# Kernel tuning notes

Hardware: AMD Instinct MI355X
Metric: run time of the kernel (lower is better)

The kernel has to match this reference:

```python
import jax, jax.numpy as jnp
import numpy as np

N = 100000
E = 6400000
GAMMA = 1.0
SUPPORT = 0.05


def cohesion_kernel(q, h):
    # piecewise Akinci cohesion kernel (Cd normalization is unused in the original)
    qm1_3_q3 = (q - 1.0) ** 3 * q ** 3
    k1 = 128.0 * qm1_3_q3 + 1.0   # q <= 0.5
    k2 = 64.0 * qm1_3_q3           # q > 0.5
    return -jnp.where(q <= 0.5, k1, k2)


def kernel_gradient(q, dist, h):
    # 2D Wendland C2 kernel gradient: W = 7/(pi h^2) (1-q)^4 (1+4q)
    C = 7.0 / (np.pi * h ** 2)
    dWdq = C * (-20.0 * q * jnp.clip(1.0 - q, 0.0, None) ** 3) / h
    return dWdq[:, None] * dist  # [E,2]


def setup_inputs() -> dict:
    key = jax.random.key(0)
    k1, k2, k3, k4, k5, k6, k7 = jax.random.split(key, 7)
    neighbors = jnp.stack([
        jax.random.randint(k1, (E,), 0, N),
        jax.random.randint(k2, (E,), 0, N),
    ], axis=0)  # [2,E] int
    fluidAreas = jax.random.uniform(k3, (N,), dtype=jnp.float32)
    fluidDensities = jax.random.uniform(k4, (N,), dtype=jnp.float32) + 0.5  # avoid div-by-0
    fluidRestDensity = jax.random.uniform(k5, (N,), dtype=jnp.float32) + 0.5
    fluidRadialDistances = jax.random.uniform(k6, (E,), dtype=jnp.float32)  # q in [0,1]
    fluidDistances = jax.random.normal(k7, (E, 2), dtype=jnp.float32)
    # normalize to unit direction vectors as in the SPH pipeline
    fluidDistances = fluidDistances / (jnp.linalg.norm(fluidDistances, axis=1, keepdims=True) + 1e-7)
    return {
        'neighbors': neighbors,
        'fluidAreas': fluidAreas,
        'fluidDensities': fluidDensities,
        'fluidRestDensity': fluidRestDensity,
        'fluidRadialDistances': fluidRadialDistances,
        'fluidDistances': fluidDistances,
    }


def reference(neighbors, fluidAreas, fluidDensities, fluidRestDensity,
              fluidRadialDistances, fluidDistances):
    i = neighbors[0]
    j = neighbors[1]

    # computeNormalFunction
    fac_n = fluidAreas[j] / fluidDensities[j]                  # [E]
    grad = kernel_gradient(fluidRadialDistances, fluidDistances, SUPPORT)  # [E,2]
    normals = SUPPORT * jax.ops.segment_sum(fac_n[:, None] * grad, i, num_segments=N)  # [N,2]

    # computeCurvatureForce
    curvature = -GAMMA * jax.ops.segment_sum(normals[i] - normals[j], i, num_segments=N)

    # computeCohesionForce
    fac_c = fluidAreas[j] * fluidRestDensity[j]                # [E]
    kern = cohesion_kernel(fluidRadialDistances, SUPPORT)      # [E]
    cohesion = -GAMMA * jax.ops.segment_sum((fac_c * kern)[:, None] * fluidDistances, i, num_segments=N)

    # both forces are accumulated into fluidAcceleration
    return curvature + cohesion
```

## Files before the change

### kernel.cpp

```cpp
#include <hip/hip_runtime.h>

constexpr int N_PART = 100000;
constexpr int N_EDGE = 6400000;
constexpr float SUPPORT = 0.05f;
constexpr float PI_F = 3.14159265358979323846f;

constexpr int CH_LOG2 = 12;
constexpr int CH      = 1 << CH_LOG2;
constexpr int NCH     = (N_EDGE + CH - 1) / CH;
constexpr int BIN_LOG2 = 12;
constexpr int BINSZ   = 1 << BIN_LOG2;
constexpr int NBIN    = (N_PART + BINSZ - 1) / BINSZ;
constexpr int BT_STRIDE = 32;
constexpr int G_MAX   = 40;
constexpr int ST_NW   = 8;
constexpr int MAXC    = 272;

__global__ __launch_bounds__(512) void prep_fac(
    const float* __restrict__ areas,
    const float* __restrict__ dens,
    const float* __restrict__ rest,
    float2* __restrict__ fac)
{
    int p = blockIdx.x * blockDim.x + threadIdx.x;
    if (p < N_PART)
        fac[p] = make_float2(areas[p] / dens[p], areas[p] * rest[p]);
}

__global__ __launch_bounds__(512) void l1_sort(
    const int* __restrict__ nb,
    const float2* __restrict__ fac,
    const float* __restrict__ q,
    const float2* __restrict__ dist,
    unsigned* __restrict__ gpack,
    float2* __restrict__ gpay1,
    float2* __restrict__ gpay2,
    unsigned* __restrict__ btab)
{
    __shared__ unsigned rec_pack[CH];
    __shared__ float    rec_q[CH];
    __shared__ float    rec_dx[CH];
    __shared__ float    rec_dy[CH];
    __shared__ unsigned hist[ST_NW * NBIN];
    __shared__ unsigned wbase[ST_NW * NBIN];
    __shared__ unsigned kpre[ST_NW * 8 * NBIN];
    __shared__ unsigned base[NBIN + 1];
    __shared__ unsigned bcnt[NBIN];

    const int t   = blockIdx.x;
    const int c0  = t * CH;
    const int len = min(CH, N_EDGE - c0);
    const int tid = threadIdx.x;
    const int wid = tid >> 6;
    const int lane = tid & 63;

    unsigned iv[8], jv[8];
    float    qv[8], dxv[8], dyv[8];
    #pragma unroll
    for (int k = 0; k < 8; ++k) {
        int idx = tid + k * 512;
        if (idx < len) {
            iv[k] = (unsigned)nb[c0 + idx];
            jv[k] = (unsigned)nb[N_EDGE + c0 + idx];
            qv[k] = q[c0 + idx];
            float2 d = dist[c0 + idx];
            dxv[k] = d.x;
            dyv[k] = d.y;
        }
    }

    unsigned rnk[8];
    unsigned cntb = 0;
    #pragma unroll
    for (int k = 0; k < 8; ++k) {
        int idx = tid + k * 512;
        unsigned bin = (idx < len) ? (iv[k] >> BIN_LOG2) : 0xFFu;
        if (lane < NBIN) kpre[(wid * 8 + k) * NBIN + lane] = cntb;
        unsigned r = 0;
        for (unsigned b = 0; b < (unsigned)NBIN; ++b) {
            unsigned long long m = __ballot(bin == b);
            unsigned lt = __builtin_amdgcn_mbcnt_hi((unsigned)(m >> 32),
                          __builtin_amdgcn_mbcnt_lo((unsigned)m, 0u));
            if (bin == b) r = lt;
            if ((unsigned)lane == b) cntb += (unsigned)__popcll(m);
        }
        rnk[k] = r;
    }
    if (lane < NBIN) hist[wid * NBIN + lane] = cntb;
    __syncthreads();

    if (tid < NBIN) {
        unsigned run = 0;
        for (int w = 0; w < ST_NW; ++w) {
            wbase[w * NBIN + tid] = run;
            run += hist[w * NBIN + tid];
        }
        bcnt[tid] = run;
    }
    __syncthreads();
    if (tid == 0) {
        unsigned run = 0;
        for (int b = 0; b < NBIN; ++b) { base[b] = run; run += bcnt[b]; }
        base[NBIN] = run;
    }
    __syncthreads();
    if (tid < ST_NW * NBIN) wbase[tid] += base[tid % NBIN];
    if (tid < NBIN)  btab[t * BT_STRIDE + tid]  = base[tid];
    if (tid == NBIN) btab[t * BT_STRIDE + NBIN] = (unsigned)len;
    __syncthreads();

    #pragma unroll
    for (int k = 0; k < 8; ++k) {
        int idx = tid + k * 512;
        if (idx < len) {
            unsigned i   = iv[k];
            unsigned bin = i >> BIN_LOG2;
            unsigned pos = (wbase[wid * NBIN + bin]
                          + kpre[(wid * 8 + k) * NBIN + bin]
                          + rnk[k]) & (CH - 1);
            rec_pack[pos] = ((i & (BINSZ - 1)) << 17) | jv[k];
            rec_q[pos]    = qv[k];
            rec_dx[pos]   = dxv[k];
            rec_dy[pos]   = dyv[k];
        }
    }
    __syncthreads();

    const float Cw = 7.0f / (PI_F * SUPPORT * SUPPORT);
    for (int p = tid; p < len; p += 512) {
        unsigned pack = rec_pack[p];
        float qq = rec_q[p];
        float dx = rec_dx[p], dy = rec_dy[p];
        unsigned j = pack & 0x1FFFFu;
        float2 f = fac[j];

        float omq  = fmaxf(1.0f - qq, 0.0f);
        float dWdq = Cw * (-20.0f * qq * omq * omq * omq) * (1.0f / SUPPORT);
        float s    = SUPPORT * f.x * dWdq;

        float qm1  = qq - 1.0f;
        float tt   = qm1 * qm1 * qm1 * qq * qq * qq;
        float kern = (qq <= 0.5f) ? fmaf(128.0f, tt, 1.0f) : 64.0f * tt;
        float fc   = f.y * kern;

        int o = c0 + p;
        gpack[o] = pack;
        gpay1[o] = make_float2(s * dx, s * dy);
        gpay2[o] = make_float2(fc * dx, fc * dy);
    }
}

__global__ __launch_bounds__(512) void passB(
    const unsigned* __restrict__ btab,
    const unsigned* __restrict__ gpack,
    const float2* __restrict__ gpay1,
    float2* __restrict__ partials,
    int G)
{
    __shared__ float accx[BINSZ];
    __shared__ float accy[BINSZ];
    __shared__ unsigned s_sb[MAXC], s_se[MAXC];
    const int b = blockIdx.x % NBIN;
    const int g = blockIdx.x / NBIN;
    const int wave = threadIdx.x >> 6;
    const int lane = threadIdx.x & 63;

    const int t0 = (int)((long long)g * NCH / G);
    const int t1 = (int)((long long)(g + 1) * NCH / G);
    const int nt = t1 - t0;

    for (int k = threadIdx.x; k < BINSZ; k += 512) { accx[k] = 0.0f; accy[k] = 0.0f; }
    for (int c = threadIdx.x; c < nt; c += 512) {
        s_sb[c] = btab[(t0 + c) * BT_STRIDE + b];
        s_se[c] = btab[(t0 + c) * BT_STRIDE + b + 1];
    }
    __syncthreads();

    for (int c = wave; c < nt; c += 8) {
        const int c0  = (t0 + c) * CH;
        unsigned sb = s_sb[c], se = s_se[c];
        unsigned k = sb + lane;
        for (; k + 64 < se; k += 128) {
            int o0 = c0 + (int)k, o1 = o0 + 64;
            unsigned pk0 = gpack[o0], pk1 = gpack[o1];
            float2 p0 = gpay1[o0], p1 = gpay1[o1];
            unsigned l0 = (pk0 >> 17) & (BINSZ - 1);
            unsigned l1 = (pk1 >> 17) & (BINSZ - 1);
            atomicAdd(&accx[l0], p0.x);
            atomicAdd(&accy[l0], p0.y);
            atomicAdd(&accx[l1], p1.x);
            atomicAdd(&accy[l1], p1.y);
        }
        if (k < se) {
            int o = c0 + (int)k;
            unsigned pk = gpack[o];
            float2 p = gpay1[o];
            unsigned loc = (pk >> 17) & (BINSZ - 1);
            atomicAdd(&accx[loc], p.x);
            atomicAdd(&accy[loc], p.y);
        }
    }
    __syncthreads();

    float2* __restrict__ dst = partials + (size_t)g * (NBIN * BINSZ) + (size_t)b * BINSZ;
    for (int k = threadIdx.x; k < BINSZ; k += 512)
        dst[k] = make_float2(accx[k], accy[k]);
}

__global__ __launch_bounds__(512) void passD(
    const unsigned* __restrict__ btab,
    const unsigned* __restrict__ gpack,
    const float2* __restrict__ gpay2,
    const float2* __restrict__ normals,
    float2* __restrict__ partials,
    int G)
{
    __shared__ float accx[BINSZ];
    __shared__ float accy[BINSZ];
    __shared__ unsigned s_sb[MAXC], s_se[MAXC];
    const int b = blockIdx.x % NBIN;
    const int g = blockIdx.x / NBIN;
    const int wave = threadIdx.x >> 6;
    const int lane = threadIdx.x & 63;

    const int t0 = (int)((long long)g * NCH / G);
    const int t1 = (int)((long long)(g + 1) * NCH / G);
    const int nt = t1 - t0;

    for (int k = threadIdx.x; k < BINSZ; k += 512) { accx[k] = 0.0f; accy[k] = 0.0f; }
    for (int c = threadIdx.x; c < nt; c += 512) {
        s_sb[c] = btab[(t0 + c) * BT_STRIDE + b];
        s_se[c] = btab[(t0 + c) * BT_STRIDE + b + 1];
    }
    __syncthreads();

    const int gbase = b * BINSZ;
    for (int c = wave; c < nt; c += 8) {
        const int c0  = (t0 + c) * CH;
        unsigned sb = s_sb[c], se = s_se[c];
        unsigned k = sb + lane;
        for (; k + 64 < se; k += 128) {
            int o0 = c0 + (int)k, o1 = o0 + 64;
            unsigned pk0 = gpack[o0], pk1 = gpack[o1];
            float2 h0 = gpay2[o0], h1 = gpay2[o1];
            unsigned j0 = min(pk0 & 0x1FFFFu, (unsigned)(N_PART - 1));
            unsigned j1 = min(pk1 & 0x1FFFFu, (unsigned)(N_PART - 1));
            unsigned l0 = (pk0 >> 17) & (BINSZ - 1);
            unsigned l1 = (pk1 >> 17) & (BINSZ - 1);
            unsigned i0 = min((unsigned)(gbase + l0), (unsigned)(N_PART - 1));
            unsigned i1 = min((unsigned)(gbase + l1), (unsigned)(N_PART - 1));
            float2 nj0 = normals[j0];
            float2 nj1 = normals[j1];
            float2 ni0 = normals[i0];
            float2 ni1 = normals[i1];
            atomicAdd(&accx[l0], nj0.x - ni0.x + h0.x);
            atomicAdd(&accy[l0], nj0.y - ni0.y + h0.y);
            atomicAdd(&accx[l1], nj1.x - ni1.x + h1.x);
            atomicAdd(&accy[l1], nj1.y - ni1.y + h1.y);
        }
        if (k < se) {
            int o = c0 + (int)k;
            unsigned pk = gpack[o];
            float2 coh = gpay2[o];
            unsigned j   = min(pk & 0x1FFFFu, (unsigned)(N_PART - 1));
            unsigned loc = (pk >> 17) & (BINSZ - 1);
            unsigned ii  = min((unsigned)(gbase + loc), (unsigned)(N_PART - 1));
            float2 nj = normals[j];
            float2 ni = normals[ii];
            atomicAdd(&accx[loc], nj.x - ni.x + coh.x);
            atomicAdd(&accy[loc], nj.y - ni.y + coh.y);
        }
    }
    __syncthreads();

    float2* __restrict__ dst = partials + (size_t)g * (NBIN * BINSZ) + (size_t)b * BINSZ;
    for (int k = threadIdx.x; k < BINSZ; k += 512)
        dst[k] = make_float2(accx[k], accy[k]);
}

__global__ __launch_bounds__(256) void reduceG(
    const float2* __restrict__ partials, float2* __restrict__ dst, int G)
{
    int p = blockIdx.x * blockDim.x + threadIdx.x;
    if (p >= N_PART) return;
    float ax = 0.0f, ay = 0.0f;
    for (int g = 0; g < G; ++g) {
        float2 v = partials[(size_t)g * (NBIN * BINSZ) + p];
        ax += v.x; ay += v.y;
    }
    dst[p] = make_float2(ax, ay);
}

constexpr int FB_BSZ_LOG2 = 13;
constexpr int FB_BSZ   = 1 << FB_BSZ_LOG2;
constexpr int FB_NBINS = (N_PART + FB_BSZ - 1) / FB_BSZ;
constexpr int FB_NP_PAD = FB_NBINS * FB_BSZ;
constexpr int FB_C_TARGET = 39;

__global__ __launch_bounds__(1024) void fb_pass1_binned(
    const int* __restrict__ nb, const float* __restrict__ areas,
    const float* __restrict__ dens, const float* __restrict__ q,
    const float2* __restrict__ dist, float* __restrict__ partials, int C)
{
    __shared__ float lds[2 * FB_BSZ];
    const int b = blockIdx.x % FB_NBINS;
    const int c = blockIdx.x / FB_NBINS;
    for (int k = threadIdx.x; k < 2 * FB_BSZ; k += blockDim.x) lds[k] = 0.0f;
    __syncthreads();
    const int start = (int)((long long)c       * (N_EDGE / 4) / C) * 4;
    const int end   = (int)((long long)(c + 1) * (N_EDGE / 4) / C) * 4;
    const int4* __restrict__ nb4 = (const int4*)nb;
    const float Cw = 7.0f / (PI_F * SUPPORT * SUPPORT);
    for (int e = start + (int)threadIdx.x * 4; e < end; e += (int)blockDim.x * 4) {
        int4 iq = nb4[e >> 2];
        #pragma unroll
        for (int k = 0; k < 4; ++k) {
            int iv = (k == 0) ? iq.x : (k == 1) ? iq.y : (k == 2) ? iq.z : iq.w;
            if ((iv >> FB_BSZ_LOG2) == b) {
                int ee = e + k;
                int j  = nb[N_EDGE + ee];
                float qq  = q[ee];
                float fac = areas[j] / dens[j];
                float omq  = fmaxf(1.0f - qq, 0.0f);
                float dWdq = Cw * (-20.0f * qq * omq * omq * omq) * (1.0f / SUPPORT);
                float s = SUPPORT * fac * dWdq;
                float2 d = dist[ee];
                int loc = (iv & (FB_BSZ - 1)) << 1;
                atomicAdd(&lds[loc],     s * d.x);
                atomicAdd(&lds[loc + 1], s * d.y);
            }
        }
    }
    __syncthreads();
    float2* __restrict__ dst = (float2*)partials + (size_t)c * FB_NP_PAD + (size_t)b * FB_BSZ;
    const float2* __restrict__ src = (const float2*)lds;
    for (int k = threadIdx.x; k < FB_BSZ; k += blockDim.x) dst[k] = src[k];
}

__global__ __launch_bounds__(1024) void fb_pass2_binned(
    const int* __restrict__ nb, const float* __restrict__ areas,
    const float* __restrict__ rest, const float* __restrict__ q,
    const float2* __restrict__ dist, const float2* __restrict__ normals,
    float* __restrict__ partials, int C)
{
    __shared__ float lds[2 * FB_BSZ];
    const int b = blockIdx.x % FB_NBINS;
    const int c = blockIdx.x / FB_NBINS;
    for (int k = threadIdx.x; k < 2 * FB_BSZ; k += blockDim.x) lds[k] = 0.0f;
    __syncthreads();
    const int start = (int)((long long)c       * (N_EDGE / 4) / C) * 4;
    const int end   = (int)((long long)(c + 1) * (N_EDGE / 4) / C) * 4;
    const int4* __restrict__ nb4 = (const int4*)nb;
    for (int e = start + (int)threadIdx.x * 4; e < end; e += (int)blockDim.x * 4) {
        int4 iq = nb4[e >> 2];
        #pragma unroll
        for (int k = 0; k < 4; ++k) {
            int iv = (k == 0) ? iq.x : (k == 1) ? iq.y : (k == 2) ? iq.z : iq.w;
            if ((iv >> FB_BSZ_LOG2) == b) {
                int ee = e + k;
                int j  = nb[N_EDGE + ee];
                float2 ni = normals[iv];
                float2 nj = normals[j];
                float qq  = q[ee];
                float fc  = areas[j] * rest[j];
                float qm1 = qq - 1.0f;
                float t   = qm1 * qm1 * qm1 * qq * qq * qq;
                float kern = (qq <= 0.5f) ? fmaf(128.0f, t, 1.0f) : 64.0f * t;
                float2 d = dist[ee];
                int loc = (iv & (FB_BSZ - 1)) << 1;
                atomicAdd(&lds[loc],     -(ni.x - nj.x) + fc * kern * d.x);
                atomicAdd(&lds[loc + 1], -(ni.y - nj.y) + fc * kern * d.y);
            }
        }
    }
    __syncthreads();
    float2* __restrict__ dst = (float2*)partials + (size_t)c * FB_NP_PAD + (size_t)b * FB_BSZ;
    const float2* __restrict__ src = (const float2*)lds;
    for (int k = threadIdx.x; k < FB_BSZ; k += blockDim.x) dst[k] = src[k];
}

__global__ __launch_bounds__(256) void fb_reduce_partials(
    const float* __restrict__ partials, float* __restrict__ dst, int C)
{
    int p = blockIdx.x * blockDim.x + threadIdx.x;
    if (p >= N_PART) return;
    const float2* __restrict__ p2 = (const float2*)partials;
    float ax = 0.0f, ay = 0.0f;
    for (int c = 0; c < C; ++c) {
        float2 v = p2[(size_t)c * FB_NP_PAD + p];
        ax += v.x; ay += v.y;
    }
    ((float2*)dst)[p] = make_float2(ax, ay);
}

__global__ __launch_bounds__(256) void fb_zero2(float* __restrict__ a,
                                                float* __restrict__ b, int n) {
    int idx = blockIdx.x * blockDim.x + threadIdx.x;
    if (idx < n) { a[idx] = 0.0f; b[idx] = 0.0f; }
}

__global__ __launch_bounds__(256) void fb_pass1_atomic(
    const int* __restrict__ nb, const float* __restrict__ areas,
    const float* __restrict__ dens, const float* __restrict__ q,
    const float2* __restrict__ dist, float* __restrict__ normals)
{
    int e = blockIdx.x * blockDim.x + threadIdx.x;
    if (e >= N_EDGE) return;
    int i = nb[e];
    int j = nb[N_EDGE + e];
    float qq  = q[e];
    float fac = areas[j] / dens[j];
    const float Cw = 7.0f / (PI_F * SUPPORT * SUPPORT);
    float omq  = fmaxf(1.0f - qq, 0.0f);
    float dWdq = Cw * (-20.0f * qq * omq * omq * omq) * (1.0f / SUPPORT);
    float s = SUPPORT * fac * dWdq;
    float2 d = dist[e];
    atomicAdd(&normals[2 * i],     s * d.x);
    atomicAdd(&normals[2 * i + 1], s * d.y);
}

__global__ __launch_bounds__(256) void fb_pass2_atomic(
    const int* __restrict__ nb, const float* __restrict__ areas,
    const float* __restrict__ rest, const float* __restrict__ q,
    const float2* __restrict__ dist, const float2* __restrict__ normals,
    float* __restrict__ out)
{
    int e = blockIdx.x * blockDim.x + threadIdx.x;
    if (e >= N_EDGE) return;
    int i = nb[e];
    int j = nb[N_EDGE + e];
    float2 ni = normals[i];
    float2 nj = normals[j];
    float qq  = q[e];
    float fc  = areas[j] * rest[j];
    float qm1 = qq - 1.0f;
    float t   = qm1 * qm1 * qm1 * qq * qq * qq;
    float kern = (qq <= 0.5f) ? fmaf(128.0f, t, 1.0f) : 64.0f * t;
    float2 d = dist[e];
    atomicAdd(&out[2 * i],     -(ni.x - nj.x) + fc * kern * d.x);
    atomicAdd(&out[2 * i + 1], -(ni.y - nj.y) + fc * kern * d.y);
}

extern "C" void kernel_launch(void* const* d_in, const int* in_sizes, int n_in,
                              void* d_out, int out_size, void* d_ws, size_t ws_size,
                              hipStream_t stream) {
    const int*   nb    = (const int*)d_in[0];
    const float* areas = (const float*)d_in[1];
    const float* dens  = (const float*)d_in[2];
    const float* rest  = (const float*)d_in[3];
    const float* q     = (const float*)d_in[4];
    const float* dist  = (const float*)d_in[5];
    float* out = (float*)d_out;

    size_t off = 0;
    auto take = [&](size_t bytes) { size_t o = off; off += (bytes + 255) & ~(size_t)255; return o; };
    size_t o_pack    = take((size_t)N_EDGE * sizeof(unsigned));
    size_t o_pay1    = take((size_t)N_EDGE * sizeof(float2));
    size_t o_pay2    = take((size_t)N_EDGE * sizeof(float2));
    size_t o_btab    = take((size_t)NCH * BT_STRIDE * sizeof(unsigned));
    size_t o_normals = take((size_t)N_PART * sizeof(float2));
    size_t o_fac     = take((size_t)N_PART * sizeof(float2));
    size_t base_need = off;
    const size_t per_g = (size_t)(NBIN * BINSZ) * sizeof(float2);

    int G = 0;
    if (ws_size > base_need) {
        G = (int)((ws_size - base_need) / per_g);
        if (G > G_MAX) G = G_MAX;
    }

    char* ws = (char*)d_ws;

    if (G >= 6) {
        unsigned* gpack   = (unsigned*)(ws + o_pack);
        float2*   gpay1   = (float2*)(ws + o_pay1);
        float2*   gpay2   = (float2*)(ws + o_pay2);
        unsigned* btab    = (unsigned*)(ws + o_btab);
        float2*   normals = (float2*)(ws + o_normals);
        float2*   fac     = (float2*)(ws + o_fac);
        float2*   partials= (float2*)(ws + base_need);

        prep_fac<<<(N_PART + 511) / 512, 512, 0, stream>>>(areas, dens, rest, fac);
        l1_sort<<<NCH, 512, 0, stream>>>(
            nb, fac, q, (const float2*)dist,
            gpack, gpay1, gpay2, btab);
        passB<<<NBIN * G, 512, 0, stream>>>(btab, gpack, gpay1, partials, G);
        reduceG<<<(N_PART + 255) / 256, 256, 0, stream>>>(partials, normals, G);
        passD<<<NBIN * G, 512, 0, stream>>>(btab, gpack, gpay2, normals, partials, G);
        reduceG<<<(N_PART + 255) / 256, 256, 0, stream>>>(partials, (float2*)out, G);
        return;
    }

    const size_t normals_pad = 1 << 20;
    float* normals  = (float*)d_ws;
    float* partials = (float*)((char*)d_ws + normals_pad);
    const size_t per_chunk = (size_t)FB_NP_PAD * 2 * sizeof(float);
    int C = 0;
    if (ws_size > normals_pad) {
        C = (int)((ws_size - normals_pad) / per_chunk);
        if (C > FB_C_TARGET) C = FB_C_TARGET;
    }

    if (C >= 4) {
        const int grid = FB_NBINS * C;
        fb_pass1_binned<<<grid, 1024, 0, stream>>>(
            nb, areas, dens, q, (const float2*)dist, partials, C);
        fb_reduce_partials<<<(N_PART + 255) / 256, 256, 0, stream>>>(partials, normals, C);
        fb_pass2_binned<<<grid, 1024, 0, stream>>>(
            nb, areas, rest, q, (const float2*)dist, (const float2*)normals, partials, C);
        fb_reduce_partials<<<(N_PART + 255) / 256, 256, 0, stream>>>(partials, out, C);
    } else {
        const int nv = 2 * N_PART;
        fb_zero2<<<(nv + 255) / 256, 256, 0, stream>>>(normals, out, nv);
        const int blocks = (N_EDGE + 255) / 256;
        fb_pass1_atomic<<<blocks, 256, 0, stream>>>(
            nb, areas, dens, q, (const float2*)dist, normals);
        fb_pass2_atomic<<<blocks, 256, 0, stream>>>(
            nb, areas, rest, q, (const float2*)dist, (const float2*)normals, out);
    }
}
```

Baseline: 384.7 us.

## Use LDS atomic ranking for bin scatter and pack records as float4

The per-chunk bin sort now ranks edges with shared-memory atomic counters instead of a 25-iteration ballot/mbcnt loop per element, which drops the kpre prefix table. The four separate shared arrays for pack, q, dx and dy become one float4 array, so each record is written and read with a single 16-byte access. The pass that accumulates into bins now unrolls its loads to four per lane to keep more memory requests in flight. The atomic ranking makes the order within a bin nondeterministic, which can change the float summation order, and the atomics may contend on hot bins.

```diff
diff --git a/kernel.cpp b/kernel.cpp
--- a/kernel.cpp
+++ b/kernel.cpp
@@ -37,13 +37,9 @@
     float2* __restrict__ gpay2,
     unsigned* __restrict__ btab)
 {
-    __shared__ unsigned rec_pack[CH];
-    __shared__ float    rec_q[CH];
-    __shared__ float    rec_dx[CH];
-    __shared__ float    rec_dy[CH];
+    __shared__ float4   rec[CH];
     __shared__ unsigned hist[ST_NW * NBIN];
-    __shared__ unsigned wbase[ST_NW * NBIN];
-    __shared__ unsigned kpre[ST_NW * 8 * NBIN];
+    __shared__ unsigned curw[ST_NW * NBIN];
     __shared__ unsigned base[NBIN + 1];
     __shared__ unsigned bcnt[NBIN];
 
@@ -52,7 +48,8 @@
     const int len = min(CH, N_EDGE - c0);
     const int tid = threadIdx.x;
     const int wid = tid >> 6;
-    const int lane = tid & 63;
+
+    for (int k = tid; k < ST_NW * NBIN; k += 512) hist[k] = 0u;
 
     unsigned iv[8], jv[8];
     float    qv[8], dxv[8], dyv[8];
@@ -68,31 +65,20 @@
             dyv[k] = d.y;
         }
     }
-
-    unsigned rnk[8];
-    unsigned cntb = 0;
+    __syncthreads();
+
     #pragma unroll
     for (int k = 0; k < 8; ++k) {
         int idx = tid + k * 512;
-        unsigned bin = (idx < len) ? (iv[k] >> BIN_LOG2) : 0xFFu;
-        if (lane < NBIN) kpre[(wid * 8 + k) * NBIN + lane] = cntb;
-        unsigned r = 0;
-        for (unsigned b = 0; b < (unsigned)NBIN; ++b) {
-            unsigned long long m = __ballot(bin == b);
-            unsigned lt = __builtin_amdgcn_mbcnt_hi((unsigned)(m >> 32),
-                          __builtin_amdgcn_mbcnt_lo((unsigned)m, 0u));
-            if (bin == b) r = lt;
-            if ((unsigned)lane == b) cntb += (unsigned)__popcll(m);
-        }
-        rnk[k] = r;
-    }
-    if (lane < NBIN) hist[wid * NBIN + lane] = cntb;
+        if (idx < len)
+            atomicAdd(&hist[wid * NBIN + (iv[k] >> BIN_LOG2)], 1u);
+    }
     __syncthreads();
 
     if (tid < NBIN) {
         unsigned run = 0;
         for (int w = 0; w < ST_NW; ++w) {
-            wbase[w * NBIN + tid] = run;
+            curw[w * NBIN + tid] = run;
             run += hist[w * NBIN + tid];
         }
         bcnt[tid] = run;
@@ -104,7 +90,7 @@
         base[NBIN] = run;
     }
     __syncthreads();
-    if (tid < ST_NW * NBIN) wbase[tid] += base[tid % NBIN];
+    if (tid < ST_NW * NBIN) curw[tid] += base[tid % NBIN];
     if (tid < NBIN)  btab[t * BT_STRIDE + tid]  = base[tid];
     if (tid == NBIN) btab[t * BT_STRIDE + NBIN] = (unsigned)len;
     __syncthreads();
@@ -115,22 +101,19 @@
         if (idx < len) {
             unsigned i   = iv[k];
             unsigned bin = i >> BIN_LOG2;
-            unsigned pos = (wbase[wid * NBIN + bin]
-                          + kpre[(wid * 8 + k) * NBIN + bin]
-                          + rnk[k]) & (CH - 1);
-            rec_pack[pos] = ((i & (BINSZ - 1)) << 17) | jv[k];
-            rec_q[pos]    = qv[k];
-            rec_dx[pos]   = dxv[k];
-            rec_dy[pos]   = dyv[k];
+            unsigned r = atomicAdd(&curw[wid * NBIN + bin], 1u) & (CH - 1);
+            unsigned pk = ((i & (BINSZ - 1)) << 17) | jv[k];
+            rec[r] = make_float4(__uint_as_float(pk), qv[k], dxv[k], dyv[k]);
         }
     }
     __syncthreads();
 
     const float Cw = 7.0f / (PI_F * SUPPORT * SUPPORT);
     for (int p = tid; p < len; p += 512) {
-        unsigned pack = rec_pack[p];
-        float qq = rec_q[p];
-        float dx = rec_dx[p], dy = rec_dy[p];
+        float4 v = rec[p];
+        unsigned pack = __float_as_uint(v.x);
+        float qq = v.y;
+        float dx = v.z, dy = v.w;
         unsigned j = pack & 0x1FFFFu;
         float2 f = fac[j];
 
@@ -180,18 +163,22 @@
         const int c0  = (t0 + c) * CH;
         unsigned sb = s_sb[c], se = s_se[c];
         unsigned k = sb + lane;
-        for (; k + 64 < se; k += 128) {
-            int o0 = c0 + (int)k, o1 = o0 + 64;
-            unsigned pk0 = gpack[o0], pk1 = gpack[o1];
-            float2 p0 = gpay1[o0], p1 = gpay1[o1];
+        for (; k + 192 < se; k += 256) {
+            int o0 = c0 + (int)k;
+            unsigned pk0 = gpack[o0], pk1 = gpack[o0 + 64],
+                     pk2 = gpack[o0 + 128], pk3 = gpack[o0 + 192];
+            float2 p0 = gpay1[o0],       p1 = gpay1[o0 + 64],
+                   p2 = gpay1[o0 + 128], p3 = gpay1[o0 + 192];
             unsigned l0 = (pk0 >> 17) & (BINSZ - 1);
             unsigned l1 = (pk1 >> 17) & (BINSZ - 1);
-            atomicAdd(&accx[l0], p0.x);
-            atomicAdd(&accy[l0], p0.y);
-            atomicAdd(&accx[l1], p1.x);
-            atomicAdd(&accy[l1], p1.y);
-        }
-        if (k < se) {
+            unsigned l2 = (pk2 >> 17) & (BINSZ - 1);
+            unsigned l3 = (pk3 >> 17) & (BINSZ - 1);
+            atomicAdd(&accx[l0], p0.x);  atomicAdd(&accy[l0], p0.y);
+            atomicAdd(&accx[l1], p1.x);  atomicAdd(&accy[l1], p1.y);
+            atomicAdd(&accx[l2], p2.x);  atomicAdd(&accy[l2], p2.y);
+            atomicAdd(&accx[l3], p3.x);  atomicAdd(&accy[l3], p3.y);
+        }
+        for (; k < se; k += 64) {
             int o = c0 + (int)k;
             unsigned pk = gpack[o];
             float2 p = gpay1[o];
```

Measured after the change: 366.5 us. 4.7% less time.
